# Kernel optimization log

Hardware: AMD Instinct MI355X
Metric: run time of the kernel (lower is better)

Reference implementation:

```python
import jax, jax.numpy as jnp
import numpy as np

D_MODEL = 512
NUM_HEADS = 8
HEAD_DIM = D_MODEL // NUM_HEADS


def setup_inputs() -> dict:
    key = jax.random.key(0)
    ks = jax.random.split(key, 11)
    N, S, D = 2, 4096, D_MODEL
    s = 1.0 / np.sqrt(D)
    return {
        "query": jax.random.normal(ks[0], (N, S, D), jnp.float32),
        "key": jax.random.normal(ks[1], (N, S, D), jnp.float32),
        "value": jax.random.normal(ks[2], (N, S, D), jnp.float32),
        "Wq": jax.random.normal(ks[3], (D, D), jnp.float32) * s,
        "bq": jnp.zeros((D,), jnp.float32),
        "Wk": jax.random.normal(ks[4], (D, D), jnp.float32) * s,
        "bk": jnp.zeros((D,), jnp.float32),
        "Wv": jax.random.normal(ks[5], (D, D), jnp.float32) * s,
        "bv": jnp.zeros((D,), jnp.float32),
        "Wo": jax.random.normal(ks[6], (D, D), jnp.float32) * s,
        "bo": jnp.zeros((D,), jnp.float32),
    }


def reference(query, key, value, Wq, bq, Wk, bk, Wv, bv, Wo, bo):
    N, S, D = query.shape
    H, Hd = NUM_HEADS, HEAD_DIM
    # Linear projections (torch Linear: x @ W.T + b), split heads -> [N,H,S,Hd]
    Q = (query @ Wq.T + bq).reshape(N, S, H, Hd).transpose(0, 2, 1, 3)
    K = (key @ Wk.T + bk).reshape(N, S, H, Hd).transpose(0, 2, 1, 3)
    V = (value @ Wv.T + bv).reshape(N, S, H, Hd).transpose(0, 2, 1, 3)
    scale = 1.0 / np.sqrt(Hd)
    energy = jnp.einsum("nhqd,nhkd->nhqk", Q, K) * scale  # [N,H,S,S]
    attention = jax.nn.softmax(energy, axis=-1)
    out = jnp.einsum("nhqk,nhkd->nhqd", attention, V)
    out = out.transpose(0, 2, 1, 3).reshape(N, S, D)
    return out @ Wo.T + bo
```

## Files before the change

### kernel.cpp

```cpp
#include <hip/hip_runtime.h>


#define SEQ 4096
#define PERHEAD 262144
#define CEXPF 0.18033688011112042f

typedef short bf16x8 __attribute__((ext_vector_type(8)));
typedef short bf16x4 __attribute__((ext_vector_type(4)));
typedef float f32x4 __attribute__((ext_vector_type(4)));
typedef unsigned short u16;
typedef unsigned int u32;

__device__ inline float bf2f(u16 h) {
    return __uint_as_float(((u32)h) << 16);
}
__device__ inline u16 f2bf(float f) {
    u32 u = __float_as_uint(f);
    u = (u + 0x7fffu + ((u >> 16) & 1u)) >> 16;
    return (u16)u;
}
__device__ inline u32 packtrunc(float lo, float hi) {
    return __builtin_amdgcn_perm(__float_as_uint(hi), __float_as_uint(lo),
                                 0x07060302u);
}
__device__ inline uint4 pack8(float4 a, float4 b) {
    uint4 r;
    r.x = (u32)f2bf(a.x) | ((u32)f2bf(a.y) << 16);
    r.y = (u32)f2bf(a.z) | ((u32)f2bf(a.w) << 16);
    r.z = (u32)f2bf(b.x) | ((u32)f2bf(b.y) << 16);
    r.w = (u32)f2bf(b.z) | ((u32)f2bf(b.w) << 16);
    return r;
}

__global__ void detect_dtype(const u16* __restrict__ W, int* __restrict__ flag) {
    const int lane = threadIdx.x & 63;
    u16 u = W[2 * lane];
    int e = (u >> 7) & 0xFF;
    int plaus = (u == 0) || (e >= 100 && e <= 132);
    unsigned long long m = __ballot(plaus);
    if (lane == 0) *flag = (__popcll(m) >= 48) ? 0 : 1;
}

__global__ __launch_bounds__(256) void prep(
    const void* __restrict__ W0, const void* __restrict__ W1,
    const void* __restrict__ W2, const void* __restrict__ W3,
    const void* __restrict__ b0, const void* __restrict__ b1,
    const void* __restrict__ b2, const void* __restrict__ b3,
    u16* __restrict__ Wc, u16* __restrict__ bc, const int* __restrict__ flag)
{
    const int m = blockIdx.y;
    const void* Ws = (m == 0) ? W0 : (m == 1) ? W1 : (m == 2) ? W2 : W3;
    const void* bs = (m == 0) ? b0 : (m == 1) ? b1 : (m == 2) ? b2 : b3;
    const int isf32 = *flag;
    if (blockIdx.x < 128) {
        const int idx = blockIdx.x * 2048 + threadIdx.x * 8;
        u16* dst = Wc + (size_t)m * 262144 + idx;
        if (isf32) {
            const float4* s = (const float4*)((const float*)Ws + idx);
            *(uint4*)dst = pack8(s[0], s[1]);
        } else {
            *(uint4*)dst = *(const uint4*)((const u16*)Ws + idx);
        }
    } else if (threadIdx.x < 64) {
        const int idx = threadIdx.x * 8;
        u16* dst = bc + m * 512 + idx;
        if (isf32) {
            const float4* s = (const float4*)((const float*)bs + idx);
            *(uint4*)dst = pack8(s[0], s[1]);
        } else {
            *(uint4*)dst = *(const uint4*)((const u16*)bs + idx);
        }
    }
}

template <int A_BF16>
__device__ inline void gemm_body(
    const void* __restrict__ Av, const u16* __restrict__ B,
    const u16* __restrict__ bias, void* __restrict__ outv,
    int isf32, int mode, float scale, int m0, int n0,
    u16* As, u16* Bs)
{
    const int tid = threadIdx.x;
    const int wave = tid >> 6, lane = tid & 63, quad = lane >> 4, ln = lane & 15;
    const int qr = wave >> 1, qc = wave & 1;

    f32x4 acc[4][4];
#pragma unroll
    for (int i = 0; i < 4; i++)
#pragma unroll
        for (int j = 0; j < 4; j++) acc[i][j] = (f32x4){0.f, 0.f, 0.f, 0.f};

    const int srow = tid >> 1;
    const int scol = (tid & 1) * 16;
    const uint4*  Ag16 = (const uint4*) ((const u16*)Av + (size_t)(m0 + srow) * 512 + scol);
    const float4* Ag32 = (const float4*)((const float*)Av + (size_t)(m0 + srow) * 512 + scol);
    const uint4*  Bg   = (const uint4*) (B + (size_t)(n0 + srow) * 512 + scol);
    uint4* Al = (uint4*)(As + srow * 40 + scol);
    uint4* Bl = (uint4*)(Bs + srow * 40 + scol);

    for (int kk = 0; kk < 512; kk += 32) {
        __syncthreads();
        uint4 aw0, aw1;
        if (A_BF16 || !isf32) {
            aw0 = Ag16[0]; aw1 = Ag16[1];
            Ag16 += 4;
        } else {
            float4 f0 = Ag32[0], f1 = Ag32[1], f2 = Ag32[2], f3 = Ag32[3];
            Ag32 += 8;
            aw0 = pack8(f0, f1); aw1 = pack8(f2, f3);
        }
        uint4 bw0 = Bg[0], bw1 = Bg[1];
        Bg += 4;
        Al[0] = aw0; Al[1] = aw1; Bl[0] = bw0; Bl[1] = bw1;
        __syncthreads();
        bf16x8 af[4], bfr[4];
#pragma unroll
        for (int mi = 0; mi < 4; mi++)
            af[mi] = *(const bf16x8*)(As + (qr * 64 + mi * 16 + ln) * 40 + quad * 8);
#pragma unroll
        for (int ni = 0; ni < 4; ni++)
            bfr[ni] = *(const bf16x8*)(Bs + (qc * 64 + ni * 16 + ln) * 40 + quad * 8);
#pragma unroll
        for (int mi = 0; mi < 4; mi++)
#pragma unroll
            for (int ni = 0; ni < 4; ni++)
                acc[mi][ni] = __builtin_amdgcn_mfma_f32_16x16x32_bf16(
                    af[mi], bfr[ni], acc[mi][ni], 0, 0, 0);
    }

#pragma unroll
    for (int ni = 0; ni < 4; ni++) {
        const int col = n0 + qc * 64 + ni * 16 + ln;
        const float bvv = bf2f(bias[col]);
#pragma unroll
        for (int mi = 0; mi < 4; mi++) {
#pragma unroll
            for (int r = 0; r < 4; r++) {
                const int row = m0 + qr * 64 + mi * 16 + quad * 4 + r;
                const float v = (acc[mi][ni][r] + bvv) * scale;
                if (mode == 0) {
                    const size_t idx = (size_t)row * 512 + col;
                    if (isf32) ((float*)outv)[idx] = v;
                    else       ((u16*)outv)[idx] = f2bf(v);
                } else {
                    const int b = row >> 12, s = row & 4095;
                    const int h = col >> 6, hd = col & 63;
                    size_t idx;
                    if (mode == 1)
                        idx = (size_t)(b * 8 + h) * PERHEAD + (size_t)s * 64 + hd;
                    else
                        idx = (size_t)(b * 8 + h) * PERHEAD + (size_t)hd * 4096 + s;
                    ((u16*)outv)[idx] = f2bf(v);
                }
            }
        }
    }
}

__global__ __launch_bounds__(256) void qkv_proj(
    const void* __restrict__ q, const void* __restrict__ k, const void* __restrict__ v,
    const u16* __restrict__ Wc, const u16* __restrict__ bc,
    u16* __restrict__ Qh, u16* __restrict__ Kh, u16* __restrict__ Vt,
    const int* __restrict__ flag)
{
    __shared__ __align__(16) u16 As[128 * 40];
    __shared__ __align__(16) u16 Bs[128 * 40];
    const int z = blockIdx.z;
    const void* Av = (z == 0) ? q : (z == 1) ? k : v;
    void* outv = (z == 0) ? (void*)Qh : (z == 1) ? (void*)Kh : (void*)Vt;
    const int mode = (z == 2) ? 2 : 1;
    const float scale = (z == 0) ? CEXPF : 1.0f;
    gemm_body<0>(Av, Wc + (size_t)z * 262144, bc + z * 512, outv,
                 *flag, mode, scale, blockIdx.y * 128, blockIdx.x * 128, As, Bs);
}

__global__ __launch_bounds__(256) void out_proj(
    const void* __restrict__ Av, const u16* __restrict__ Wc,
    const u16* __restrict__ bc, void* __restrict__ outv,
    const int* __restrict__ flag)
{
    __shared__ __align__(16) u16 As[128 * 40];
    __shared__ __align__(16) u16 Bs[128 * 40];
    gemm_body<1>(Av, Wc + (size_t)3 * 262144, bc + 3 * 512, outv,
                 *flag, 0, 1.0f, blockIdx.y * 128, blockIdx.x * 128, As, Bs);
}

__global__ __launch_bounds__(256) void attn_kernel(
    const u16* __restrict__ Q, const u16* __restrict__ K,
    const u16* __restrict__ Vt, u16* __restrict__ AO)
{
    __shared__ __align__(16) u16 Ks[64 * 72];
    __shared__ __align__(16) u16 Vs[64 * 72];

    const int tid = threadIdx.x;
    const int w = tid >> 6, lane = tid & 63, quad = lane >> 4, ln = lane & 15;
    const int bh = blockIdx.y;
    const int q0 = blockIdx.x * 128;
    const size_t base = (size_t)bh * PERHEAD;

    bf16x8 qf[2][2];
#pragma unroll
    for (int qt = 0; qt < 2; qt++) {
        const uint4* qp = (const uint4*)(Q + base + (size_t)(q0 + w * 32 + qt * 16 + ln) * 64);
        uint4 v0 = qp[quad], v1 = qp[4 + quad];
        qf[qt][0] = *(bf16x8*)&v0;
        qf[qt][1] = *(bf16x8*)&v1;
    }

    bf16x8 ones;
#pragma unroll
    for (int j = 0; j < 8; j++) ones[j] = (short)0x3F80;

    f32x4 oT[2][4];
    f32x4 lacc[2];
#pragma unroll
    for (int qt = 0; qt < 2; qt++) {
        lacc[qt] = (f32x4){0.f, 0.f, 0.f, 0.f};
#pragma unroll
        for (int mt = 0; mt < 4; mt++) oT[qt][mt] = (f32x4){0.f, 0.f, 0.f, 0.f};
    }

    const int srow = tid >> 2;
    const int sc = (tid & 3) * 16;
    const uint4* Kg = (const uint4*)(K + base + (size_t)srow * 64 + sc);
    const uint4* Vg = (const uint4*)(Vt + base + (size_t)srow * 4096 + sc);
    uint4* Kl = (uint4*)(Ks + srow * 72 + sc);
    uint4* Vl = (uint4*)(Vs + srow * 72 + sc);

    for (int k0 = 0; k0 < SEQ; k0 += 64) {
        __syncthreads();
        {
            uint4 a = Kg[0], b = Kg[1], c = Vg[0], d = Vg[1];
            Kg += 512;
            Vg += 8;
            Kl[0] = a; Kl[1] = b; Vl[0] = c; Vl[1] = d;
        }
        __syncthreads();

        f32x4 s[2][4];
#pragma unroll
        for (int t = 0; t < 2; t++)
#pragma unroll
            for (int kt = 0; kt < 4; kt++) {
                bf16x8 kf = *(const bf16x8*)(Ks + (kt * 16 + ln) * 72 + t * 32 + quad * 8);
#pragma unroll
                for (int qt = 0; qt < 2; qt++) {
                    if (t == 0)
                        s[qt][kt] = __builtin_amdgcn_mfma_f32_16x16x32_bf16(
                            kf, qf[qt][0], (f32x4){0.f, 0.f, 0.f, 0.f}, 0, 0, 0);
                    else
                        s[qt][kt] = __builtin_amdgcn_mfma_f32_16x16x32_bf16(
                            kf, qf[qt][1], s[qt][kt], 0, 0, 0);
                }
            }

        bf16x8 pf[2][2];
#pragma unroll
        for (int qt = 0; qt < 2; qt++)
#pragma unroll
            for (int c = 0; c < 2; c++) {
                float e0 = exp2f(s[qt][2 * c][0]), e1 = exp2f(s[qt][2 * c][1]);
                float e2 = exp2f(s[qt][2 * c][2]), e3 = exp2f(s[qt][2 * c][3]);
                float f0 = exp2f(s[qt][2 * c + 1][0]), f1 = exp2f(s[qt][2 * c + 1][1]);
                float f2 = exp2f(s[qt][2 * c + 1][2]), f3 = exp2f(s[qt][2 * c + 1][3]);
                u32 w0 = packtrunc(e0, e1), w1 = packtrunc(e2, e3);
                u32 w2 = packtrunc(f0, f1), w3 = packtrunc(f2, f3);
                uint4 pk = {w0, w1, w2, w3};
                pf[qt][c] = *(bf16x8*)&pk;
            }

#pragma unroll
        for (int qt = 0; qt < 2; qt++)
#pragma unroll
            for (int c = 0; c < 2; c++)
                lacc[qt] = __builtin_amdgcn_mfma_f32_16x16x32_bf16(
                    ones, pf[qt][c], lacc[qt], 0, 0, 0);

#pragma unroll
        for (int c = 0; c < 2; c++)
#pragma unroll
            for (int mt = 0; mt < 4; mt++) {
                const u16* vrow = Vs + (mt * 16 + ln) * 72 + c * 32 + quad * 4;
                bf16x4 v0 = *(const bf16x4*)(vrow);
                bf16x4 v1 = *(const bf16x4*)(vrow + 16);
                bf16x8 vf;
#pragma unroll
                for (int j = 0; j < 4; j++) { vf[j] = v0[j]; vf[4 + j] = v1[j]; }
#pragma unroll
                for (int qt = 0; qt < 2; qt++)
                    oT[qt][mt] = __builtin_amdgcn_mfma_f32_16x16x32_bf16(
                        vf, pf[qt][c], oT[qt][mt], 0, 0, 0);
            }
    }

    const int b = bh >> 3, h = bh & 7;
#pragma unroll
    for (int qt = 0; qt < 2; qt++) {
        const float inv = 1.0f / lacc[qt][0];
        const int qrow = q0 + w * 32 + qt * 16 + ln;
        u16* op = AO + (size_t)(b * 4096 + qrow) * 512 + h * 64 + quad * 4;
#pragma unroll
        for (int mt = 0; mt < 4; mt++) {
            uint2 pk;
            pk.x = (u32)f2bf(oT[qt][mt][0] * inv) | ((u32)f2bf(oT[qt][mt][1] * inv) << 16);
            pk.y = (u32)f2bf(oT[qt][mt][2] * inv) | ((u32)f2bf(oT[qt][mt][3] * inv) << 16);
            *(uint2*)(op + mt * 16) = pk;
        }
    }
}

extern "C" void kernel_launch(void* const* d_in, const int* in_sizes, int n_in,
                              void* d_out, int out_size, void* d_ws, size_t ws_size,
                              hipStream_t stream)
{
    (void)in_sizes; (void)n_in; (void)out_size; (void)ws_size;
    const void* q  = d_in[0];
    const void* k  = d_in[1];
    const void* v  = d_in[2];
    const void* Wq = d_in[3];
    const void* bq = d_in[4];
    const void* Wk = d_in[5];
    const void* bk = d_in[6];
    const void* Wv = d_in[7];
    const void* bv = d_in[8];
    const void* Wo = d_in[9];
    const void* bo = d_in[10];

    u16* ws = (u16*)d_ws;
    u16* Kh = ws;
    u16* Vt = ws + 4194304;
    u16* AO = ws + 8388608;
    u16* Wc = ws + 12582912;
    u16* bc = ws + 12582912 + 1048576;
    int* flag = (int*)(ws + 12582912 + 1048576 + 2048);
    u16* Qh = (u16*)d_out;

    detect_dtype<<<1, 64, 0, stream>>>((const u16*)Wq, flag);
    prep<<<dim3(129, 4), 256, 0, stream>>>(Wq, Wk, Wv, Wo, bq, bk, bv, bo,
                                           Wc, bc, flag);
    qkv_proj<<<dim3(4, 64, 3), 256, 0, stream>>>(q, k, v, Wc, bc, Qh, Kh, Vt, flag);
    attn_kernel<<<dim3(32, 16), 256, 0, stream>>>(Qh, Kh, Vt, AO);
    out_proj<<<dim3(4, 64), 256, 0, stream>>>(AO, Wc, bc, d_out, flag);
}
```

Measured before the change: 283.4 us.

## Double-buffer LDS tiles in GEMM and attention, permute V layout for vector loads

Switches the projection GEMMs and the attention loop to double-buffered shared memory. The next tile's global loads are issued before the MFMAs on the current tile and written to the other buffer afterwards, leaving one barrier per iteration instead of two. The V-transpose write now permutes the sequence index within each 64-block, so the attention kernel can fetch a bf16x8 V fragment in one LDS load instead of two bf16x4 loads plus a shuffle. The cost is double the LDS per block, which may reduce occupancy, and the prefetched data is held in registers across the compute.

```diff
diff --git a/kernel.cpp b/kernel.cpp
--- a/kernel.cpp
+++ b/kernel.cpp
@@ -6,7 +6,6 @@
 #define CEXPF 0.18033688011112042f
 
 typedef short bf16x8 __attribute__((ext_vector_type(8)));
-typedef short bf16x4 __attribute__((ext_vector_type(4)));
 typedef float f32x4 __attribute__((ext_vector_type(4)));
 typedef unsigned short u16;
 typedef unsigned int u32;
@@ -95,37 +94,58 @@
     const uint4*  Ag16 = (const uint4*) ((const u16*)Av + (size_t)(m0 + srow) * 512 + scol);
     const float4* Ag32 = (const float4*)((const float*)Av + (size_t)(m0 + srow) * 512 + scol);
     const uint4*  Bg   = (const uint4*) (B + (size_t)(n0 + srow) * 512 + scol);
-    uint4* Al = (uint4*)(As + srow * 40 + scol);
-    uint4* Bl = (uint4*)(Bs + srow * 40 + scol);
+    const int lofs = srow * 40 + scol;
+
+    uint4 aw0, aw1, bw0, bw1;
+    if (A_BF16 || !isf32) {
+        aw0 = Ag16[0]; aw1 = Ag16[1]; Ag16 += 4;
+    } else {
+        float4 f0 = Ag32[0], f1 = Ag32[1], f2 = Ag32[2], f3 = Ag32[3];
+        Ag32 += 8;
+        aw0 = pack8(f0, f1); aw1 = pack8(f2, f3);
+    }
+    bw0 = Bg[0]; bw1 = Bg[1]; Bg += 4;
+    {
+        uint4* Al = (uint4*)(As + lofs);
+        uint4* Bl = (uint4*)(Bs + lofs);
+        Al[0] = aw0; Al[1] = aw1; Bl[0] = bw0; Bl[1] = bw1;
+    }
+    __syncthreads();
 
     for (int kk = 0; kk < 512; kk += 32) {
-        __syncthreads();
-        uint4 aw0, aw1;
-        if (A_BF16 || !isf32) {
-            aw0 = Ag16[0]; aw1 = Ag16[1];
-            Ag16 += 4;
-        } else {
-            float4 f0 = Ag32[0], f1 = Ag32[1], f2 = Ag32[2], f3 = Ag32[3];
-            Ag32 += 8;
-            aw0 = pack8(f0, f1); aw1 = pack8(f2, f3);
-        }
-        uint4 bw0 = Bg[0], bw1 = Bg[1];
-        Bg += 4;
-        Al[0] = aw0; Al[1] = aw1; Bl[0] = bw0; Bl[1] = bw1;
-        __syncthreads();
+        const int cur = (kk >> 5) & 1;
+        const bool more = (kk + 32) < 512;
+        if (more) {
+            if (A_BF16 || !isf32) {
+                aw0 = Ag16[0]; aw1 = Ag16[1]; Ag16 += 4;
+            } else {
+                float4 f0 = Ag32[0], f1 = Ag32[1], f2 = Ag32[2], f3 = Ag32[3];
+                Ag32 += 8;
+                aw0 = pack8(f0, f1); aw1 = pack8(f2, f3);
+            }
+            bw0 = Bg[0]; bw1 = Bg[1]; Bg += 4;
+        }
+        const u16* Ab = As + cur * 5120;
+        const u16* Bb = Bs + cur * 5120;
         bf16x8 af[4], bfr[4];
 #pragma unroll
         for (int mi = 0; mi < 4; mi++)
-            af[mi] = *(const bf16x8*)(As + (qr * 64 + mi * 16 + ln) * 40 + quad * 8);
+            af[mi] = *(const bf16x8*)(Ab + (qr * 64 + mi * 16 + ln) * 40 + quad * 8);
 #pragma unroll
         for (int ni = 0; ni < 4; ni++)
-            bfr[ni] = *(const bf16x8*)(Bs + (qc * 64 + ni * 16 + ln) * 40 + quad * 8);
+            bfr[ni] = *(const bf16x8*)(Bb + (qc * 64 + ni * 16 + ln) * 40 + quad * 8);
 #pragma unroll
         for (int mi = 0; mi < 4; mi++)
 #pragma unroll
             for (int ni = 0; ni < 4; ni++)
                 acc[mi][ni] = __builtin_amdgcn_mfma_f32_16x16x32_bf16(
                     af[mi], bfr[ni], acc[mi][ni], 0, 0, 0);
+        if (more) {
+            uint4* Al = (uint4*)(As + (cur ^ 1) * 5120 + lofs);
+            uint4* Bl = (uint4*)(Bs + (cur ^ 1) * 5120 + lofs);
+            Al[0] = aw0; Al[1] = aw1; Bl[0] = bw0; Bl[1] = bw1;
+            __syncthreads();
+        }
     }
 
 #pragma unroll
@@ -146,10 +166,13 @@
                     const int b = row >> 12, s = row & 4095;
                     const int h = col >> 6, hd = col & 63;
                     size_t idx;
-                    if (mode == 1)
+                    if (mode == 1) {
                         idx = (size_t)(b * 8 + h) * PERHEAD + (size_t)s * 64 + hd;
-                    else
-                        idx = (size_t)(b * 8 + h) * PERHEAD + (size_t)hd * 4096 + s;
+                    } else {
+                        const int sp = (s & ~63) | (s & 32) | ((s & 12) << 1)
+                                     | ((s & 16) >> 2) | (s & 3);
+                        idx = (size_t)(b * 8 + h) * PERHEAD + (size_t)hd * 4096 + sp;
+                    }
                     ((u16*)outv)[idx] = f2bf(v);
                 }
             }
@@ -163,8 +186,8 @@
     u16* __restrict__ Qh, u16* __restrict__ Kh, u16* __restrict__ Vt,
     const int* __restrict__ flag)
 {
-    __shared__ __align__(16) u16 As[128 * 40];
-    __shared__ __align__(16) u16 Bs[128 * 40];
+    __shared__ __align__(16) u16 As[2 * 128 * 40];
+    __shared__ __align__(16) u16 Bs[2 * 128 * 40];
     const int z = blockIdx.z;
     const void* Av = (z == 0) ? q : (z == 1) ? k : v;
     void* outv = (z == 0) ? (void*)Qh : (z == 1) ? (void*)Kh : (void*)Vt;
@@ -179,8 +202,8 @@
     const u16* __restrict__ bc, void* __restrict__ outv,
     const int* __restrict__ flag)
 {
-    __shared__ __align__(16) u16 As[128 * 40];
-    __shared__ __align__(16) u16 Bs[128 * 40];
+    __shared__ __align__(16) u16 As[2 * 128 * 40];
+    __shared__ __align__(16) u16 Bs[2 * 128 * 40];
     gemm_body<1>(Av, Wc + (size_t)3 * 262144, bc + 3 * 512, outv,
                  *flag, 0, 1.0f, blockIdx.y * 128, blockIdx.x * 128, As, Bs);
 }
@@ -189,8 +212,8 @@
     const u16* __restrict__ Q, const u16* __restrict__ K,
     const u16* __restrict__ Vt, u16* __restrict__ AO)
 {
-    __shared__ __align__(16) u16 Ks[64 * 72];
-    __shared__ __align__(16) u16 Vs[64 * 72];
+    __shared__ __align__(16) u16 Ks[2 * 64 * 72];
+    __shared__ __align__(16) u16 Vs[2 * 64 * 72];
 
     const int tid = threadIdx.x;
     const int w = tid >> 6, lane = tid & 63, quad = lane >> 4, ln = lane & 15;
@@ -224,25 +247,33 @@
     const int sc = (tid & 3) * 16;
     const uint4* Kg = (const uint4*)(K + base + (size_t)srow * 64 + sc);
     const uint4* Vg = (const uint4*)(Vt + base + (size_t)srow * 4096 + sc);
-    uint4* Kl = (uint4*)(Ks + srow * 72 + sc);
-    uint4* Vl = (uint4*)(Vs + srow * 72 + sc);
+    const int lofs = srow * 72 + sc;
+
+    uint4 ka = Kg[0], kb = Kg[1], va = Vg[0], vb = Vg[1];
+    Kg += 512; Vg += 8;
+    {
+        uint4* Kl = (uint4*)(Ks + lofs);
+        uint4* Vl = (uint4*)(Vs + lofs);
+        Kl[0] = ka; Kl[1] = kb; Vl[0] = va; Vl[1] = vb;
+    }
+    __syncthreads();
 
     for (int k0 = 0; k0 < SEQ; k0 += 64) {
-        __syncthreads();
-        {
-            uint4 a = Kg[0], b = Kg[1], c = Vg[0], d = Vg[1];
-            Kg += 512;
-            Vg += 8;
-            Kl[0] = a; Kl[1] = b; Vl[0] = c; Vl[1] = d;
-        }
-        __syncthreads();
+        const int cur = (k0 >> 6) & 1;
+        const bool more = (k0 + 64) < SEQ;
+        if (more) {
+            ka = Kg[0]; kb = Kg[1]; va = Vg[0]; vb = Vg[1];
+            Kg += 512; Vg += 8;
+        }
+        const u16* Kb = Ks + cur * 4608;
+        const u16* Vb = Vs + cur * 4608;
 
         f32x4 s[2][4];
 #pragma unroll
         for (int t = 0; t < 2; t++)
 #pragma unroll
             for (int kt = 0; kt < 4; kt++) {
-                bf16x8 kf = *(const bf16x8*)(Ks + (kt * 16 + ln) * 72 + t * 32 + quad * 8);
+                bf16x8 kf = *(const bf16x8*)(Kb + (kt * 16 + ln) * 72 + t * 32 + quad * 8);
 #pragma unroll
                 for (int qt = 0; qt < 2; qt++) {
                     if (t == 0)
@@ -280,17 +311,19 @@
         for (int c = 0; c < 2; c++)
 #pragma unroll
             for (int mt = 0; mt < 4; mt++) {
-                const u16* vrow = Vs + (mt * 16 + ln) * 72 + c * 32 + quad * 4;
-                bf16x4 v0 = *(const bf16x4*)(vrow);
-                bf16x4 v1 = *(const bf16x4*)(vrow + 16);
-                bf16x8 vf;
-#pragma unroll
-                for (int j = 0; j < 4; j++) { vf[j] = v0[j]; vf[4 + j] = v1[j]; }
+                bf16x8 vf = *(const bf16x8*)(Vb + (mt * 16 + ln) * 72 + c * 32 + quad * 8);
 #pragma unroll
                 for (int qt = 0; qt < 2; qt++)
                     oT[qt][mt] = __builtin_amdgcn_mfma_f32_16x16x32_bf16(
                         vf, pf[qt][c], oT[qt][mt], 0, 0, 0);
             }
+
+        if (more) {
+            uint4* Kl = (uint4*)(Ks + (cur ^ 1) * 4608 + lofs);
+            uint4* Vl = (uint4*)(Vs + (cur ^ 1) * 4608 + lofs);
+            Kl[0] = ka; Kl[1] = kb; Vl[0] = va; Vl[1] = vb;
+            __syncthreads();
+        }
     }
 
     const int b = bh >> 3, h = bh & 7;
```

After: 314.8 us. 11.1% more time.

## Load K/V fragments directly from global into registers, dropping LDS staging

Applied to the files above, without the earlier changes.

The attention kernel no longer stages K and V tiles through shared memory behind two barriers per iteration. Each wave now loads its MFMA fragments straight from global memory (L2-cached), double-buffering the K fragments in registers. The V-transpose layout written by the projection kernel is permuted so each lane's 8-element V fragment is contiguous and can be read as one uint4. The grid is flattened and remapped so each head's blocks land on the same XCD for L2 locality. The cost is redundant global/L2 traffic, since every wave reads the full K and V, plus higher register pressure.

```diff
diff --git a/kernel.cpp b/kernel.cpp
--- a/kernel.cpp
+++ b/kernel.cpp
@@ -6,7 +6,6 @@
 #define CEXPF 0.18033688011112042f
 
 typedef short bf16x8 __attribute__((ext_vector_type(8)));
-typedef short bf16x4 __attribute__((ext_vector_type(4)));
 typedef float f32x4 __attribute__((ext_vector_type(4)));
 typedef unsigned short u16;
 typedef unsigned int u32;
@@ -146,10 +145,13 @@
                     const int b = row >> 12, s = row & 4095;
                     const int h = col >> 6, hd = col & 63;
                     size_t idx;
-                    if (mode == 1)
+                    if (mode == 1) {
                         idx = (size_t)(b * 8 + h) * PERHEAD + (size_t)s * 64 + hd;
-                    else
-                        idx = (size_t)(b * 8 + h) * PERHEAD + (size_t)hd * 4096 + s;
+                    } else {
+                        const int sp = (s & ~63) | (s & 32) | ((s & 12) << 1)
+                                     | ((s & 16) >> 2) | (s & 3);
+                        idx = (size_t)(b * 8 + h) * PERHEAD + (size_t)hd * 4096 + sp;
+                    }
                     ((u16*)outv)[idx] = f2bf(v);
                 }
             }
@@ -189,19 +191,18 @@
     const u16* __restrict__ Q, const u16* __restrict__ K,
     const u16* __restrict__ Vt, u16* __restrict__ AO)
 {
-    __shared__ __align__(16) u16 Ks[64 * 72];
-    __shared__ __align__(16) u16 Vs[64 * 72];
-
     const int tid = threadIdx.x;
     const int w = tid >> 6, lane = tid & 63, quad = lane >> 4, ln = lane & 15;
-    const int bh = blockIdx.y;
-    const int q0 = blockIdx.x * 128;
+    const int flat = blockIdx.x;
+    const int xcd = flat & 7, sub = flat >> 3;
+    const int bh = xcd * 2 + (sub >> 5);
+    const int q0 = (sub & 31) * 128 + w * 32;
     const size_t base = (size_t)bh * PERHEAD;
 
     bf16x8 qf[2][2];
 #pragma unroll
     for (int qt = 0; qt < 2; qt++) {
-        const uint4* qp = (const uint4*)(Q + base + (size_t)(q0 + w * 32 + qt * 16 + ln) * 64);
+        const uint4* qp = (const uint4*)(Q + base + (size_t)(q0 + qt * 16 + ln) * 64);
         uint4 v0 = qp[quad], v1 = qp[4 + quad];
         qf[qt][0] = *(bf16x8*)&v0;
         qf[qt][1] = *(bf16x8*)&v1;
@@ -220,84 +221,91 @@
         for (int mt = 0; mt < 4; mt++) oT[qt][mt] = (f32x4){0.f, 0.f, 0.f, 0.f};
     }
 
-    const int srow = tid >> 2;
-    const int sc = (tid & 3) * 16;
-    const uint4* Kg = (const uint4*)(K + base + (size_t)srow * 64 + sc);
-    const uint4* Vg = (const uint4*)(Vt + base + (size_t)srow * 4096 + sc);
-    uint4* Kl = (uint4*)(Ks + srow * 72 + sc);
-    uint4* Vl = (uint4*)(Vs + srow * 72 + sc);
-
-    for (int k0 = 0; k0 < SEQ; k0 += 64) {
-        __syncthreads();
-        {
-            uint4 a = Kg[0], b = Kg[1], c = Vg[0], d = Vg[1];
-            Kg += 512;
-            Vg += 8;
-            Kl[0] = a; Kl[1] = b; Vl[0] = c; Vl[1] = d;
-        }
-        __syncthreads();
-
-        f32x4 s[2][4];
+    const u16* Kp = K + base + (size_t)ln * 64 + quad * 8;
+    const u16* Vp = Vt + base + (size_t)ln * 4096 + quad * 8;
+
+    uint4 kfr[2][8];
+#pragma unroll
+    for (int kt = 0; kt < 4; kt++)
 #pragma unroll
         for (int t = 0; t < 2; t++)
-#pragma unroll
-            for (int kt = 0; kt < 4; kt++) {
-                bf16x8 kf = *(const bf16x8*)(Ks + (kt * 16 + ln) * 72 + t * 32 + quad * 8);
-#pragma unroll
-                for (int qt = 0; qt < 2; qt++) {
-                    if (t == 0)
-                        s[qt][kt] = __builtin_amdgcn_mfma_f32_16x16x32_bf16(
-                            kf, qf[qt][0], (f32x4){0.f, 0.f, 0.f, 0.f}, 0, 0, 0);
-                    else
-                        s[qt][kt] = __builtin_amdgcn_mfma_f32_16x16x32_bf16(
-                            kf, qf[qt][1], s[qt][kt], 0, 0, 0);
+            kfr[0][kt * 2 + t] = *(const uint4*)(Kp + kt * 1024 + t * 32);
+
+#pragma unroll 1
+    for (int k0 = 0; k0 < SEQ; k0 += 128) {
+#pragma unroll
+        for (int ph = 0; ph < 2; ph++) {
+            const int kt0 = k0 + ph * 64;
+            uint4 vfr[8];
+#pragma unroll
+            for (int mt = 0; mt < 4; mt++)
+#pragma unroll
+                for (int c = 0; c < 2; c++)
+                    vfr[mt * 2 + c] = *(const uint4*)(Vp + (size_t)mt * 65536 + kt0 + c * 32);
+#pragma unroll
+            for (int kt = 0; kt < 4; kt++)
+#pragma unroll
+                for (int t = 0; t < 2; t++)
+                    kfr[ph ^ 1][kt * 2 + t] =
+                        *(const uint4*)(Kp + (size_t)(kt0 + 64) * 64 + kt * 1024 + t * 32);
+
+            f32x4 s[2][4];
+#pragma unroll
+            for (int t = 0; t < 2; t++)
+#pragma unroll
+                for (int kt = 0; kt < 4; kt++) {
+                    bf16x8 kf = *(bf16x8*)&kfr[ph][kt * 2 + t];
+#pragma unroll
+                    for (int qt = 0; qt < 2; qt++) {
+                        if (t == 0)
+                            s[qt][kt] = __builtin_amdgcn_mfma_f32_16x16x32_bf16(
+                                kf, qf[qt][0], (f32x4){0.f, 0.f, 0.f, 0.f}, 0, 0, 0);
+                        else
+                            s[qt][kt] = __builtin_amdgcn_mfma_f32_16x16x32_bf16(
+                                kf, qf[qt][1], s[qt][kt], 0, 0, 0);
+                    }
                 }
-            }
-
-        bf16x8 pf[2][2];
-#pragma unroll
-        for (int qt = 0; qt < 2; qt++)
-#pragma unroll
-            for (int c = 0; c < 2; c++) {
-                float e0 = exp2f(s[qt][2 * c][0]), e1 = exp2f(s[qt][2 * c][1]);
-                float e2 = exp2f(s[qt][2 * c][2]), e3 = exp2f(s[qt][2 * c][3]);
-                float f0 = exp2f(s[qt][2 * c + 1][0]), f1 = exp2f(s[qt][2 * c + 1][1]);
-                float f2 = exp2f(s[qt][2 * c + 1][2]), f3 = exp2f(s[qt][2 * c + 1][3]);
-                u32 w0 = packtrunc(e0, e1), w1 = packtrunc(e2, e3);
-                u32 w2 = packtrunc(f0, f1), w3 = packtrunc(f2, f3);
-                uint4 pk = {w0, w1, w2, w3};
-                pf[qt][c] = *(bf16x8*)&pk;
-            }
-
-#pragma unroll
-        for (int qt = 0; qt < 2; qt++)
+
+            bf16x8 pf[2][2];
+#pragma unroll
+            for (int qt = 0; qt < 2; qt++)
+#pragma unroll
+                for (int c = 0; c < 2; c++) {
+                    float e0 = exp2f(s[qt][2 * c][0]), e1 = exp2f(s[qt][2 * c][1]);
+                    float e2 = exp2f(s[qt][2 * c][2]), e3 = exp2f(s[qt][2 * c][3]);
+                    float f0 = exp2f(s[qt][2 * c + 1][0]), f1 = exp2f(s[qt][2 * c + 1][1]);
+                    float f2 = exp2f(s[qt][2 * c + 1][2]), f3 = exp2f(s[qt][2 * c + 1][3]);
+                    u32 w0 = packtrunc(e0, e1), w1 = packtrunc(e2, e3);
+                    u32 w2 = packtrunc(f0, f1), w3 = packtrunc(f2, f3);
+                    uint4 pk = {w0, w1, w2, w3};
+                    pf[qt][c] = *(bf16x8*)&pk;
+                }
+
+#pragma unroll
+            for (int qt = 0; qt < 2; qt++)
+#pragma unroll
+                for (int c = 0; c < 2; c++)
+                    lacc[qt] = __builtin_amdgcn_mfma_f32_16x16x32_bf16(
+                        ones, pf[qt][c], lacc[qt], 0, 0, 0);
+
 #pragma unroll
             for (int c = 0; c < 2; c++)
-                lacc[qt] = __builtin_amdgcn_mfma_f32_16x16x32_bf16(
-                    ones, pf[qt][c], lacc[qt], 0, 0, 0);
-
-#pragma unroll
-        for (int c = 0; c < 2; c++)
-#pragma unroll
-            for (int mt = 0; mt < 4; mt++) {
-                const u16* vrow = Vs + (mt * 16 + ln) * 72 + c * 32 + quad * 4;
-                bf16x4 v0 = *(const bf16x4*)(vrow);
-                bf16x4 v1 = *(const bf16x4*)(vrow + 16);
-                bf16x8 vf;
-#pragma unroll
-                for (int j = 0; j < 4; j++) { vf[j] = v0[j]; vf[4 + j] = v1[j]; }
-#pragma unroll
-                for (int qt = 0; qt < 2; qt++)
-                    oT[qt][mt] = __builtin_amdgcn_mfma_f32_16x16x32_bf16(
-                        vf, pf[qt][c], oT[qt][mt], 0, 0, 0);
-            }
+#pragma unroll
+                for (int mt = 0; mt < 4; mt++) {
+                    bf16x8 vf = *(bf16x8*)&vfr[mt * 2 + c];
+#pragma unroll
+                    for (int qt = 0; qt < 2; qt++)
+                        oT[qt][mt] = __builtin_amdgcn_mfma_f32_16x16x32_bf16(
+                            vf, pf[qt][c], oT[qt][mt], 0, 0, 0);
+                }
+        }
     }
 
     const int b = bh >> 3, h = bh & 7;
 #pragma unroll
     for (int qt = 0; qt < 2; qt++) {
         const float inv = 1.0f / lacc[qt][0];
-        const int qrow = q0 + w * 32 + qt * 16 + ln;
+        const int qrow = q0 + qt * 16 + ln;
         u16* op = AO + (size_t)(b * 4096 + qrow) * 512 + h * 64 + quad * 4;
 #pragma unroll
         for (int mt = 0; mt < 4; mt++) {
@@ -339,6 +347,6 @@
     prep<<<dim3(129, 4), 256, 0, stream>>>(Wq, Wk, Wv, Wo, bq, bk, bv, bo,
                                            Wc, bc, flag);
     qkv_proj<<<dim3(4, 64, 3), 256, 0, stream>>>(q, k, v, Wc, bc, Qh, Kh, Vt, flag);
-    attn_kernel<<<dim3(32, 16), 256, 0, stream>>>(Qh, Kh, Vt, AO);
+    attn_kernel<<<512, 256, 0, stream>>>(Qh, Kh, Vt, AO);
     out_proj<<<dim3(4, 64), 256, 0, stream>>>(AO, Wc, bc, d_out, flag);
 }
```

After: 396.2 us. +39.8%, slower.

## Permute V layout for vector LDS reads, remap attention blocks to XCDs, narrow out_proj tiles

Applied to the files above, without the earlier changes.

The V projection epilogue now stores sequence positions in a permuted order. This lets the attention kernel load each V fragment with one 16-byte LDS read instead of two 8-byte reads plus shuffles. The attention grid is flattened and remapped so that every block for a given batch-head lands on the same XCD, which should improve L2 reuse of K and V. The output projection uses 128x64 tiles, doubling its block count to fill more CUs. The trade-off is more total A-tile loads and a less regular V store pattern.

```diff
diff --git a/kernel.cpp b/kernel.cpp
--- a/kernel.cpp
+++ b/kernel.cpp
@@ -6,7 +6,6 @@
 #define CEXPF 0.18033688011112042f
 
 typedef short bf16x8 __attribute__((ext_vector_type(8)));
-typedef short bf16x4 __attribute__((ext_vector_type(4)));
 typedef float f32x4 __attribute__((ext_vector_type(4)));
 typedef unsigned short u16;
 typedef unsigned int u32;
@@ -73,7 +72,7 @@
     }
 }
 
-template <int A_BF16>
+template <int A_BF16, int NTILE>
 __device__ inline void gemm_body(
     const void* __restrict__ Av, const u16* __restrict__ B,
     const u16* __restrict__ bias, void* __restrict__ outv,
@@ -82,11 +81,14 @@
 {
     const int tid = threadIdx.x;
     const int wave = tid >> 6, lane = tid & 63, quad = lane >> 4, ln = lane & 15;
-    const int qr = wave >> 1, qc = wave & 1;
-
-    f32x4 acc[4][4];
-#pragma unroll
-    for (int i = 0; i < 4; i++)
+    constexpr int MI = (NTILE == 128) ? 4 : 2;
+    const int qr = (NTILE == 128) ? (wave >> 1) : wave;
+    const int qc = (NTILE == 128) ? (wave & 1) : 0;
+    const int rowbase = (NTILE == 128) ? qr * 64 : qr * 32;
+
+    f32x4 acc[MI][4];
+#pragma unroll
+    for (int i = 0; i < MI; i++)
 #pragma unroll
         for (int j = 0; j < 4; j++) acc[i][j] = (f32x4){0.f, 0.f, 0.f, 0.f};
 
@@ -97,6 +99,7 @@
     const uint4*  Bg   = (const uint4*) (B + (size_t)(n0 + srow) * 512 + scol);
     uint4* Al = (uint4*)(As + srow * 40 + scol);
     uint4* Bl = (uint4*)(Bs + srow * 40 + scol);
+    const bool bload = (NTILE == 128) || (tid < 128);
 
     for (int kk = 0; kk < 512; kk += 32) {
         __syncthreads();
@@ -109,19 +112,23 @@
             Ag32 += 8;
             aw0 = pack8(f0, f1); aw1 = pack8(f2, f3);
         }
-        uint4 bw0 = Bg[0], bw1 = Bg[1];
-        Bg += 4;
-        Al[0] = aw0; Al[1] = aw1; Bl[0] = bw0; Bl[1] = bw1;
+        uint4 bw0, bw1;
+        if (bload) {
+            bw0 = Bg[0]; bw1 = Bg[1];
+            Bg += 4;
+        }
+        Al[0] = aw0; Al[1] = aw1;
+        if (bload) { Bl[0] = bw0; Bl[1] = bw1; }
         __syncthreads();
-        bf16x8 af[4], bfr[4];
-#pragma unroll
-        for (int mi = 0; mi < 4; mi++)
-            af[mi] = *(const bf16x8*)(As + (qr * 64 + mi * 16 + ln) * 40 + quad * 8);
+        bf16x8 af[MI], bfr[4];
+#pragma unroll
+        for (int mi = 0; mi < MI; mi++)
+            af[mi] = *(const bf16x8*)(As + (rowbase + mi * 16 + ln) * 40 + quad * 8);
 #pragma unroll
         for (int ni = 0; ni < 4; ni++)
             bfr[ni] = *(const bf16x8*)(Bs + (qc * 64 + ni * 16 + ln) * 40 + quad * 8);
 #pragma unroll
-        for (int mi = 0; mi < 4; mi++)
+        for (int mi = 0; mi < MI; mi++)
 #pragma unroll
             for (int ni = 0; ni < 4; ni++)
                 acc[mi][ni] = __builtin_amdgcn_mfma_f32_16x16x32_bf16(
@@ -133,10 +140,10 @@
         const int col = n0 + qc * 64 + ni * 16 + ln;
         const float bvv = bf2f(bias[col]);
 #pragma unroll
-        for (int mi = 0; mi < 4; mi++) {
+        for (int mi = 0; mi < MI; mi++) {
 #pragma unroll
             for (int r = 0; r < 4; r++) {
-                const int row = m0 + qr * 64 + mi * 16 + quad * 4 + r;
+                const int row = m0 + rowbase + mi * 16 + quad * 4 + r;
                 const float v = (acc[mi][ni][r] + bvv) * scale;
                 if (mode == 0) {
                     const size_t idx = (size_t)row * 512 + col;
@@ -146,10 +153,13 @@
                     const int b = row >> 12, s = row & 4095;
                     const int h = col >> 6, hd = col & 63;
                     size_t idx;
-                    if (mode == 1)
+                    if (mode == 1) {
                         idx = (size_t)(b * 8 + h) * PERHEAD + (size_t)s * 64 + hd;
-                    else
-                        idx = (size_t)(b * 8 + h) * PERHEAD + (size_t)hd * 4096 + s;
+                    } else {
+                        const int sp = (s & ~63) | (s & 32) | ((s & 12) << 1)
+                                     | ((s & 16) >> 2) | (s & 3);
+                        idx = (size_t)(b * 8 + h) * PERHEAD + (size_t)hd * 4096 + sp;
+                    }
                     ((u16*)outv)[idx] = f2bf(v);
                 }
             }
@@ -170,8 +180,8 @@
     void* outv = (z == 0) ? (void*)Qh : (z == 1) ? (void*)Kh : (void*)Vt;
     const int mode = (z == 2) ? 2 : 1;
     const float scale = (z == 0) ? CEXPF : 1.0f;
-    gemm_body<0>(Av, Wc + (size_t)z * 262144, bc + z * 512, outv,
-                 *flag, mode, scale, blockIdx.y * 128, blockIdx.x * 128, As, Bs);
+    gemm_body<0, 128>(Av, Wc + (size_t)z * 262144, bc + z * 512, outv,
+                      *flag, mode, scale, blockIdx.y * 128, blockIdx.x * 128, As, Bs);
 }
 
 __global__ __launch_bounds__(256) void out_proj(
@@ -180,9 +190,9 @@
     const int* __restrict__ flag)
 {
     __shared__ __align__(16) u16 As[128 * 40];
-    __shared__ __align__(16) u16 Bs[128 * 40];
-    gemm_body<1>(Av, Wc + (size_t)3 * 262144, bc + 3 * 512, outv,
-                 *flag, 0, 1.0f, blockIdx.y * 128, blockIdx.x * 128, As, Bs);
+    __shared__ __align__(16) u16 Bs[64 * 40];
+    gemm_body<1, 64>(Av, Wc + (size_t)3 * 262144, bc + 3 * 512, outv,
+                     *flag, 0, 1.0f, blockIdx.y * 128, blockIdx.x * 64, As, Bs);
 }
 
 __global__ __launch_bounds__(256) void attn_kernel(
@@ -194,8 +204,9 @@
 
     const int tid = threadIdx.x;
     const int w = tid >> 6, lane = tid & 63, quad = lane >> 4, ln = lane & 15;
-    const int bh = blockIdx.y;
-    const int q0 = blockIdx.x * 128;
+    const int xcd = blockIdx.x & 7, sub = blockIdx.x >> 3;
+    const int bh = xcd * 2 + (sub >> 5);
+    const int q0 = (sub & 31) * 128;
     const size_t base = (size_t)bh * PERHEAD;
 
     bf16x8 qf[2][2];
@@ -280,12 +291,7 @@
         for (int c = 0; c < 2; c++)
 #pragma unroll
             for (int mt = 0; mt < 4; mt++) {
-                const u16* vrow = Vs + (mt * 16 + ln) * 72 + c * 32 + quad * 4;
-                bf16x4 v0 = *(const bf16x4*)(vrow);
-                bf16x4 v1 = *(const bf16x4*)(vrow + 16);
-                bf16x8 vf;
-#pragma unroll
-                for (int j = 0; j < 4; j++) { vf[j] = v0[j]; vf[4 + j] = v1[j]; }
+                bf16x8 vf = *(const bf16x8*)(Vs + (mt * 16 + ln) * 72 + c * 32 + quad * 8);
 #pragma unroll
                 for (int qt = 0; qt < 2; qt++)
                     oT[qt][mt] = __builtin_amdgcn_mfma_f32_16x16x32_bf16(
@@ -339,6 +345,6 @@
     prep<<<dim3(129, 4), 256, 0, stream>>>(Wq, Wk, Wv, Wo, bq, bk, bv, bo,
                                            Wc, bc, flag);
     qkv_proj<<<dim3(4, 64, 3), 256, 0, stream>>>(q, k, v, Wc, bc, Qh, Kh, Vt, flag);
-    attn_kernel<<<dim3(32, 16), 256, 0, stream>>>(Qh, Kh, Vt, AO);
-    out_proj<<<dim3(4, 64), 256, 0, stream>>>(AO, Wc, bc, d_out, flag);
-}
+    attn_kernel<<<512, 256, 0, stream>>>(Qh, Kh, Vt, AO);
+    out_proj<<<dim3(8, 64), 256, 0, stream>>>(AO, Wc, bc, d_out, flag);
+}
```

New measurement: 284.4 us. About the same (+0.4%).
